# Kernel tuning notes

Measured on AMD Instinct MI355X. Metric: run time of the kernel, lower is better.

The kernel has to match this reference:

```python
import jax, jax.numpy as jnp
import numpy as np

B, S, E = 4, 2048, 768
H = 12
D = E // H  # 64

def setup_inputs() -> dict:
    key = jax.random.key(0)
    k_x, k_wqkv, k_wproj = jax.random.split(key, 3)
    x = jax.random.normal(k_x, (B, S, E), dtype=jnp.float32)
    w_qkv = jax.random.normal(k_wqkv, (E, 3 * E), dtype=jnp.float32) * 0.02
    b_qkv = jnp.zeros((3 * E,), dtype=jnp.float32)
    w_proj = jax.random.normal(k_wproj, (E, E), dtype=jnp.float32) * 0.02
    b_proj = jnp.zeros((E,), dtype=jnp.float32)
    return {"x": x, "w_qkv": w_qkv, "b_qkv": b_qkv, "w_proj": w_proj, "b_proj": b_proj}

def reference(x, w_qkv, b_qkv, w_proj, b_proj):
    # fused QKV projection: [B,S,E] -> [B,S,3E]
    qkv = jnp.einsum("bse,ef->bsf", x, w_qkv) + b_qkv
    qkv = qkv.reshape(B, S, 3, H, D)
    q, k, v = qkv[:, :, 0], qkv[:, :, 1], qkv[:, :, 2]  # [B,S,H,D]
    scale = 1.0 / jnp.sqrt(jnp.asarray(D, dtype=x.dtype))
    # causal scaled dot-product attention (explicit score matrix, as in module)
    scores = jnp.einsum("bshd,bthd->bhst", q, k) * scale  # [B,H,S,S]
    causal = jnp.tril(jnp.ones((S, S), dtype=bool))
    scores = jnp.where(causal, scores, jnp.finfo(scores.dtype).min)
    probs = jax.nn.softmax(scores, axis=-1)
    attn = jnp.einsum("bhst,bthd->bshd", probs, v).reshape(B, S, E)
    # output projection
    out = jnp.einsum("bse,ef->bsf", attn, w_proj) + b_proj
    return out
```

## Files before the change

### kernel.cpp

```cpp
#include <hip/hip_runtime.h>

#define SDIM 2048
#define EDIM 768
#define HDIM 12
#define DDIM 64
#define BDIM 4
#define MROWS (BDIM * SDIM)
#define NQKV (3 * EDIM)
#define NBH (BDIM * HDIM)
#define NTILE 32
#define NPAIR 16

typedef __attribute__((ext_vector_type(8))) short s16x8;
typedef __attribute__((ext_vector_type(4))) float f32x4;
typedef __attribute__((ext_vector_type(2))) unsigned int u32x2;

__device__ __forceinline__ short f2b(float x) {
  union { float f; unsigned u; } v; v.f = x;
  unsigned r = v.u + 0x7fffu + ((v.u >> 16) & 1u);
  return (short)(r >> 16);
}

__device__ __forceinline__ unsigned cvtpk(float lo, float hi) {
  unsigned r;
  asm volatile("v_cvt_pk_bf16_f32 %0, %1, %2" : "=v"(r) : "v"(lo), "v"(hi));
  return r;
}

__device__ __forceinline__ float fexp2(float x) {
  float r;
  asm("v_exp_f32 %0, %1" : "=v"(r) : "v"(x));
  return r;
}

__device__ __forceinline__ void gld16(const void* g, void* l) {
  __builtin_amdgcn_global_load_lds(
      (const __attribute__((address_space(1))) unsigned int*)g,
      (__attribute__((address_space(3))) unsigned int*)l, 16, 0, 0);
}

__global__ __launch_bounds__(256) void preproc(
    const float* __restrict__ x, const float* __restrict__ wqkv,
    const float* __restrict__ wproj, short* __restrict__ xb,
    short* __restrict__ wqkvt, short* __restrict__ wprojt) {
  int bid = blockIdx.x;
  if (bid < 1536) {
    int i = bid * 256 + threadIdx.x;
    const int n4 = MROWS * EDIM / 4;
    for (; i < n4; i += 1536 * 256) {
      float4 v = ((const float4*)x)[i];
      short4 o;
      o.x = f2b(v.x); o.y = f2b(v.y); o.z = f2b(v.z); o.w = f2b(v.w);
      ((short4*)xb)[i] = o;
    }
    return;
  }
  const float* in; short* out; int K, N, t;
  if (bid < 1536 + 1728) { t = bid - 1536; in = wqkv; out = wqkvt; K = EDIM; N = NQKV; }
  else { t = bid - 1536 - 1728; in = wproj; out = wprojt; K = EDIM; N = EDIM; }
  const int ntx = N / 32;
  int n0 = (t % ntx) * 32, k0 = (t / ntx) * 32;
  __shared__ float tb[32][33];
  int tx = threadIdx.x & 31, ty = threadIdx.x >> 5;
#pragma unroll
  for (int i = 0; i < 4; ++i)
    tb[ty + 8 * i][tx] = in[(size_t)(k0 + ty + 8 * i) * N + n0 + tx];
  __syncthreads();
#pragma unroll
  for (int i = 0; i < 4; ++i)
    out[(size_t)(n0 + ty + 8 * i) * K + k0 + tx] = f2b(tb[tx][ty + 8 * i]);
}

__global__ __launch_bounds__(256) void gemm_qkv(
    const short* __restrict__ A, const short* __restrict__ Bt,
    const float* __restrict__ bias, short* __restrict__ qout,
    short* __restrict__ kout, short* __restrict__ vout) {
  __shared__ char lds[3][16384];
  const int tid = threadIdx.x;
  const int l = tid & 63, w = tid >> 6;
  const int lr = l & 15, g = l >> 4;
  const int K = EDIM;

  const int chunk = gridDim.x >> 3;
  const int sid = (blockIdx.x & 7) * chunk + (blockIdx.x >> 3);
  const int ntx = NQKV >> 7;
  const int bm = (sid / ntx) * 128, bn = (sid % ntx) * 128;
  const int wm = w >> 1, wn = w & 1;

  const int srow = w * 32 + (l >> 2);
  const int sc8 = (((l & 3) ^ ((l >> 3) & 3)) << 3);
  const short* Ap0 = A + (size_t)(bm + srow) * K + sc8;
  const short* Bp0 = Bt + (size_t)(bn + srow) * K + sc8;

  f32x4 acc[4][4];
  const f32x4 z4 = {0.f, 0.f, 0.f, 0.f};
#pragma unroll
  for (int m = 0; m < 4; ++m)
#pragma unroll
    for (int n = 0; n < 4; ++n) acc[m][n] = z4;

#define STAGE(dst, t)                          \
  {                                            \
    char* Ad = (dst) + w * 2048;               \
    const short* Ap = Ap0 + (t) * 32;          \
    const short* Bp = Bp0 + (t) * 32;          \
    gld16(Ap, Ad);                             \
    gld16(Ap + 16 * K, Ad + 1024);             \
    gld16(Bp, Ad + 8192);                      \
    gld16(Bp + 16 * K, Ad + 9216);             \
  }

  const int nt = K >> 5;
  STAGE(lds[0], 0);
  STAGE(lds[1], 1);
  asm volatile("s_waitcnt vmcnt(4)" ::: "memory");
  __builtin_amdgcn_s_barrier();

  const int swz = ((lr >> 1) & 3) << 4;
  int bc = 0;
  for (int t = 0; t < nt; ++t) {
    if (t + 2 < nt) {
      int bs = bc + 2; if (bs >= 3) bs -= 3;
      STAGE(lds[bs], t + 2);
    }
    const char* Ab = lds[bc];
    const char* Bb = lds[bc] + 8192;
    s16x8 af[4], bfr[4];
#pragma unroll
    for (int m = 0; m < 4; ++m)
      af[m] = *(const s16x8*)(Ab + (wm * 64 + m * 16 + lr) * 64 + ((g << 4) ^ swz));
#pragma unroll
    for (int n = 0; n < 4; ++n)
      bfr[n] = *(const s16x8*)(Bb + (wn * 64 + n * 16 + lr) * 64 + ((g << 4) ^ swz));
    __builtin_amdgcn_s_setprio(1);
#pragma unroll
    for (int m = 0; m < 4; ++m)
#pragma unroll
      for (int n = 0; n < 4; ++n)
        acc[m][n] = __builtin_amdgcn_mfma_f32_16x16x32_bf16(af[m], bfr[n],
                                                            acc[m][n], 0, 0, 0);
    __builtin_amdgcn_s_setprio(0);
    if (t + 2 < nt) {
      asm volatile("s_waitcnt vmcnt(4)" ::: "memory");
      __builtin_amdgcn_s_barrier();
    } else if (t + 1 < nt) {
      asm volatile("s_waitcnt vmcnt(0)" ::: "memory");
      __builtin_amdgcn_s_barrier();
    }
    if (++bc == 3) bc = 0;
  }
#undef STAGE

#pragma unroll
  for (int m = 0; m < 4; ++m) {
    int rbase = bm + wm * 64 + m * 16 + g * 4;
#pragma unroll
    for (int n = 0; n < 4; ++n) {
      int col = bn + wn * 64 + n * 16 + lr;
      float bv = bias[col];
      int which = (col >= 1536) ? 2 : (col >= 768 ? 1 : 0);
      int rem = col - which * 768;
      int h = rem >> 6, d = rem & 63;
#pragma unroll
      for (int i = 0; i < 4; ++i) {
        int r = rbase + i;
        int bb = r >> 11, s = r & 2047;
        short o = f2b(acc[m][n][i] + bv);
        size_t bh = (size_t)bb * HDIM + h;
        if (which == 0)      qout[(bh * SDIM + s) * DDIM + d] = o;
        else if (which == 1) kout[(bh * SDIM + s) * DDIM + d] = o;
        else                 vout[(bh * DDIM + d) * SDIM + s] = o;
      }
    }
  }
}

__global__ __launch_bounds__(256) void gemm_proj(
    const short* __restrict__ A, const short* __restrict__ Bt,
    const float* __restrict__ bias, int M, int N, int K,
    float* __restrict__ fout) {
  __shared__ char lds[3][16384];
  const int tid = threadIdx.x;
  const int l = tid & 63, w = tid >> 6;
  const int lr = l & 15, g = l >> 4;

  const int chunk = gridDim.x >> 3;
  const int sid = (blockIdx.x & 7) * chunk + (blockIdx.x >> 3);
  const int ntx = N >> 7;
  const int bm = (sid / ntx) * 128, bn = (sid % ntx) * 128;
  const int wm = w >> 1, wn = w & 1;

  const int srow = w * 32 + (l >> 2);
  const int sc8 = (((l & 3) ^ ((l >> 3) & 3)) << 3);
  const short* Ap0 = A + (size_t)(bm + srow) * K + sc8;
  const short* Bp0 = Bt + (size_t)(bn + srow) * K + sc8;

  f32x4 acc[4][4];
  const f32x4 z4 = {0.f, 0.f, 0.f, 0.f};
#pragma unroll
  for (int m = 0; m < 4; ++m)
#pragma unroll
    for (int n = 0; n < 4; ++n) acc[m][n] = z4;

#define STAGE(dst, t)                          \
  {                                            \
    char* Ad = (dst) + w * 2048;               \
    const short* Ap = Ap0 + (t) * 32;          \
    const short* Bp = Bp0 + (t) * 32;          \
    gld16(Ap, Ad);                             \
    gld16(Ap + 16 * K, Ad + 1024);             \
    gld16(Bp, Ad + 8192);                      \
    gld16(Bp + 16 * K, Ad + 9216);             \
  }

  const int nt = K >> 5;
  STAGE(lds[0], 0);
  STAGE(lds[1], 1);
  asm volatile("s_waitcnt vmcnt(4)" ::: "memory");
  __builtin_amdgcn_s_barrier();

  const int swz = ((lr >> 1) & 3) << 4;
  int bc = 0;
  for (int t = 0; t < nt; ++t) {
    if (t + 2 < nt) {
      int bs = bc + 2; if (bs >= 3) bs -= 3;
      STAGE(lds[bs], t + 2);
    }
    const char* Ab = lds[bc];
    const char* Bb = lds[bc] + 8192;
    s16x8 af[4], bfr[4];
#pragma unroll
    for (int m = 0; m < 4; ++m)
      af[m] = *(const s16x8*)(Ab + (wm * 64 + m * 16 + lr) * 64 + ((g << 4) ^ swz));
#pragma unroll
    for (int n = 0; n < 4; ++n)
      bfr[n] = *(const s16x8*)(Bb + (wn * 64 + n * 16 + lr) * 64 + ((g << 4) ^ swz));
    __builtin_amdgcn_s_setprio(1);
#pragma unroll
    for (int m = 0; m < 4; ++m)
#pragma unroll
      for (int n = 0; n < 4; ++n)
        acc[m][n] = __builtin_amdgcn_mfma_f32_16x16x32_bf16(af[m], bfr[n],
                                                            acc[m][n], 0, 0, 0);
    __builtin_amdgcn_s_setprio(0);
    if (t + 2 < nt) {
      asm volatile("s_waitcnt vmcnt(4)" ::: "memory");
      __builtin_amdgcn_s_barrier();
    } else if (t + 1 < nt) {
      asm volatile("s_waitcnt vmcnt(0)" ::: "memory");
      __builtin_amdgcn_s_barrier();
    }
    if (++bc == 3) bc = 0;
  }
#undef STAGE

#pragma unroll
  for (int m = 0; m < 4; ++m) {
    int rbase = bm + wm * 64 + m * 16 + g * 4;
#pragma unroll
    for (int n = 0; n < 4; ++n) {
      int col = bn + wn * 64 + n * 16 + lr;
      float bv = bias[col];
#pragma unroll
      for (int i = 0; i < 4; ++i)
        fout[(size_t)(rbase + i) * N + col] = acc[m][n][i] + bv;
    }
  }
}

__global__ __launch_bounds__(256, 3) void attn_mfma4(
    const short* __restrict__ qb, const short* __restrict__ kb,
    const short* __restrict__ vb, short* __restrict__ ao) {
  __shared__ short kvbuf[2][8192];
  __shared__ short pstrip[4][1024];

  const int tid = threadIdx.x;
  const int l = tid & 63, w = tid >> 6;
  const int lr = l & 15, g = l >> 4;
  const int swz = (lr & 7) << 4;

  const int lin = blockIdx.x;
  const int xcd = lin & 7;
  const int idx = lin >> 3;
  const int bh = xcd * 6 + (idx >> 4);
  const int pair = idx & 15;
  const int tiles[2] = {NTILE - 1 - pair, pair};

  const int b = bh / HDIM, h = bh % HDIM;
  const size_t base = (size_t)bh * SDIM * DDIM;

  const int srow = w * 16 + (l >> 3);
  const int sc = (l & 7) ^ (srow & 7);
  const size_t koff0 = (size_t)srow * DDIM + sc * 8;
  const size_t koff1 = (size_t)(srow + 8) * DDIM + sc * 8;
  const size_t voff0 = (size_t)srow * SDIM + sc * 8;
  const size_t voff1 = (size_t)(srow + 8) * SDIM + sc * 8;

  const float SC = 0.125f * 1.4426950408889634f;
  char* sw = (char*)pstrip[w];

#define KVSTAGE(buf_, kt_)                                        \
  {                                                               \
    char* kd = (char*)kvbuf[buf_] + w * 2048;                     \
    const short* kp = kb + base + (size_t)(kt_) * 64 * DDIM;      \
    const short* vp = vb + base + (size_t)(kt_) * 64;             \
    gld16(kp + koff0, kd);                                        \
    gld16(kp + koff1, kd + 1024);                                 \
    gld16(vp + voff0, kd + 8192);                                 \
    gld16(vp + voff1, kd + 9216);                                 \
  }

  for (int half = 0; half < 2; ++half) {
    const int tile = tiles[half];
    const int q0w = tile * 64 + w * 16;

    s16x8 qa[2];
#pragma unroll
    for (int s = 0; s < 2; ++s)
      qa[s] = *(const s16x8*)(qb + base + (size_t)(q0w + lr) * DDIM + s * 32 + g * 8);

    const f32x4 z4 = {0.f, 0.f, 0.f, 0.f};
    f32x4 acco[4];
#pragma unroll
    for (int nd = 0; nd < 4; ++nd) acco[nd] = z4;
    float mrun = -1e30f, lsum = 0.f;

    KVSTAGE(0, 0);
    {
      const int t1 = (tile >= 1) ? 1 : 0;
      KVSTAGE(1, t1);
    }

    for (int kt = 0; kt <= tile; ++kt) {
      if (kt < tile) asm volatile("s_waitcnt vmcnt(4)" ::: "memory");
      else           asm volatile("s_waitcnt vmcnt(0)" ::: "memory");
      __builtin_amdgcn_s_barrier();

      const char* Kb = (const char*)kvbuf[kt & 1];
      const char* Vb = Kb + 8192;

      f32x4 sacc[4];
#pragma unroll
      for (int nt = 0; nt < 4; ++nt) sacc[nt] = z4;
      __builtin_amdgcn_s_setprio(1);
#pragma unroll
      for (int s = 0; s < 2; ++s)
#pragma unroll
        for (int nt = 0; nt < 4; ++nt) {
          s16x8 kf = *(const s16x8*)(Kb + nt * 2048 + lr * 128 +
                                     ((s * 64 + g * 16) ^ swz));
          sacc[nt] = __builtin_amdgcn_mfma_f32_16x16x32_bf16(kf, qa[s],
                                                             sacc[nt], 0, 0, 0);
        }
      __builtin_amdgcn_s_setprio(0);

      if (kt == tile) {
        const int rloc = w * 16 + lr;
#pragma unroll
        for (int nt = 0; nt < 4; ++nt)
#pragma unroll
          for (int i = 0; i < 4; ++i)
            if (nt * 16 + g * 4 + i > rloc) sacc[nt][i] = -1e30f;
      }

      float t0 = fmaxf(fmaxf(sacc[0][0], sacc[0][1]), fmaxf(sacc[0][2], sacc[0][3]));
      float t1 = fmaxf(fmaxf(sacc[1][0], sacc[1][1]), fmaxf(sacc[1][2], sacc[1][3]));
      float t2 = fmaxf(fmaxf(sacc[2][0], sacc[2][1]), fmaxf(sacc[2][2], sacc[2][3]));
      float t3 = fmaxf(fmaxf(sacc[3][0], sacc[3][1]), fmaxf(sacc[3][2], sacc[3][3]));
      float pmax = fmaxf(fmaxf(t0, t1), fmaxf(t2, t3));
      pmax = fmaxf(pmax, __shfl_xor(pmax, 16, 64));
      pmax = fmaxf(pmax, __shfl_xor(pmax, 32, 64));

      if (__any(pmax > mrun + 44.0f)) {
        float nm = fmaxf(mrun, pmax);
        float al = fexp2((mrun - nm) * SC);
        lsum *= al;
#pragma unroll
        for (int nd = 0; nd < 4; ++nd)
#pragma unroll
          for (int i = 0; i < 4; ++i) acco[nd][i] *= al;
        mrun = nm;
      }

      const float msc = mrun * SC;
#pragma unroll
      for (int nt = 0; nt < 4; ++nt) {
        float p0 = fexp2(__builtin_fmaf(sacc[nt][0], SC, -msc));
        float p1 = fexp2(__builtin_fmaf(sacc[nt][1], SC, -msc));
        float p2 = fexp2(__builtin_fmaf(sacc[nt][2], SC, -msc));
        float p3 = fexp2(__builtin_fmaf(sacc[nt][3], SC, -msc));
        lsum += (p0 + p1) + (p2 + p3);
        u32x2 pk = {cvtpk(p0, p1), cvtpk(p2, p3)};
        *(u32x2*)(sw + lr * 128 + (((nt * 32 + g * 8) ^ swz))) = pk;
      }

      __builtin_amdgcn_s_setprio(1);
#pragma unroll
      for (int s = 0; s < 2; ++s) {
        s16x8 pf = *(const s16x8*)(sw + lr * 128 + ((s * 64 + g * 16) ^ swz));
#pragma unroll
        for (int nd = 0; nd < 4; ++nd) {
          s16x8 vf = *(const s16x8*)(Vb + nd * 2048 + lr * 128 +
                                     ((s * 64 + g * 16) ^ swz));
          acco[nd] = __builtin_amdgcn_mfma_f32_16x16x32_bf16(vf, pf,
                                                             acco[nd], 0, 0, 0);
        }
      }
      __builtin_amdgcn_s_setprio(0);

      __builtin_amdgcn_s_barrier();
      if (kt + 2 <= tile) KVSTAGE(kt & 1, kt + 2);
    }

    lsum += __shfl_xor(lsum, 16, 64);
    lsum += __shfl_xor(lsum, 32, 64);
    float inv = 1.0f / lsum;
    size_t orow = ((size_t)b * SDIM + q0w + lr) * EDIM + h * DDIM;
#pragma unroll
    for (int nd = 0; nd < 4; ++nd) {
      unsigned lo = cvtpk(acco[nd][0] * inv, acco[nd][1] * inv);
      unsigned hi = cvtpk(acco[nd][2] * inv, acco[nd][3] * inv);
      *(unsigned*)(ao + orow + nd * 16 + g * 4) = lo;
      *(unsigned*)(ao + orow + nd * 16 + g * 4 + 2) = hi;
    }
  }
#undef KVSTAGE
}

extern "C" void kernel_launch(void* const* d_in, const int* in_sizes, int n_in,
                              void* d_out, int out_size, void* d_ws,
                              size_t ws_size, hipStream_t stream) {
  const float* x = (const float*)d_in[0];
  const float* w_qkv = (const float*)d_in[1];
  const float* b_qkv = (const float*)d_in[2];
  const float* w_proj = (const float*)d_in[3];
  const float* b_proj = (const float*)d_in[4];
  float* out = (float*)d_out;

  char* p = (char*)d_ws;
  short* xb = (short*)p;      p += (size_t)MROWS * EDIM * 2;
  short* wqkvt = (short*)p;   p += (size_t)NQKV * EDIM * 2;
  short* wprojt = (short*)p;  p += (size_t)EDIM * EDIM * 2;
  short* qbuf = (short*)p;    p += (size_t)NBH * SDIM * DDIM * 2;
  short* kbuf = (short*)p;    p += (size_t)NBH * SDIM * DDIM * 2;
  short* vbuf = (short*)p;    p += (size_t)NBH * SDIM * DDIM * 2;
  short* aob = (short*)p;     p += (size_t)MROWS * EDIM * 2;

  dim3 blk(256);
  preproc<<<dim3(1536 + 1728 + 576), blk, 0, stream>>>(x, w_qkv, w_proj, xb,
                                                       wqkvt, wprojt);
  gemm_qkv<<<dim3((MROWS / 128) * (NQKV / 128)), blk, 0, stream>>>(
      xb, wqkvt, b_qkv, qbuf, kbuf, vbuf);
  attn_mfma4<<<dim3(NPAIR * NBH), blk, 0, stream>>>(qbuf, kbuf, vbuf, aob);
  gemm_proj<<<dim3((MROWS / 128) * (EDIM / 128)), blk, 0, stream>>>(
      aob, wprojt, b_proj, MROWS, EDIM, EDIM, out);
}
```

Before: 136.9 us.

## Rewrite QKV GEMM as 256x256 tile, 8-wave kernel with deep LDS pipeline

Replaces the 128x128, 4-wave QKV projection GEMM with a 256x256-tile kernel that runs 512 threads (8 waves), each wave computing a 128x64 sub-tile. K is staged in 64-wide steps through 128KB of LDS, with half-tile stages interleaved between MFMA phases and explicit barriers. The goal is more data reuse per loaded byte and better overlap of global loads with MFMA work. The cost is a grid of only 288 blocks at one block per CU, which may leave CUs idle or unevenly loaded. It also adds higher register pressure and many more barriers.

```diff
diff --git a/kernel.cpp b/kernel.cpp
--- a/kernel.cpp
+++ b/kernel.cpp
@@ -71,19 +71,180 @@
     out[(size_t)(n0 + ty + 8 * i) * K + k0 + tx] = f2b(tb[tx][ty + 8 * i]);
 }
 
-__global__ __launch_bounds__(256) void gemm_qkv(
+__global__ __launch_bounds__(512, 1) void gemm_qkv8(
     const short* __restrict__ A, const short* __restrict__ Bt,
     const float* __restrict__ bias, short* __restrict__ qout,
     short* __restrict__ kout, short* __restrict__ vout) {
+  __shared__ char lds[131072];
+  const int tid = threadIdx.x;
+  const int l = tid & 63;
+  const int w = tid >> 6;
+  const int lr = l & 15, g = l >> 4;
+  const int K = EDIM;
+  const int nt = K >> 6;
+  const int nh = nt << 2;
+
+  const int chunk = gridDim.x >> 3;
+  const int sid = (blockIdx.x & 7) * chunk + (blockIdx.x >> 3);
+  const int ntx = NQKV >> 8;
+  const int bm = (sid / ntx) << 8;
+  const int bn = (sid % ntx) << 8;
+  const int wm = w >> 2, wn = w & 3;
+
+  const int srow = tid >> 2;
+  const int sck = ((tid & 3) ^ ((tid >> 3) & 3)) << 3;
+  const short* Ab = A + (size_t)(bm + srow) * K + sck;
+  const short* Bb = Bt + (size_t)(bn + srow) * K + sck;
+  char* dst0 = lds + tid * 16;
+
+#define STAGEH(i)                                                     \
+  {                                                                   \
+    char* d_ = dst0 + ((i) & 7) * 16384;                              \
+    const short* s_ = (((i) & 1) ? Bb : Ab) + ((i) >> 2) * 64 +       \
+                      (((i) >> 1) & 1) * 32;                          \
+    gld16(s_, d_);                                                    \
+    gld16(s_ + 128 * K, d_ + 8192);                                   \
+  }
+
+  f32x4 acc[8][4];
+  const f32x4 z4 = {0.f, 0.f, 0.f, 0.f};
+#pragma unroll
+  for (int mf = 0; mf < 8; ++mf)
+#pragma unroll
+    for (int nf = 0; nf < 4; ++nf) acc[mf][nf] = z4;
+
+  STAGEH(0); STAGEH(1); STAGEH(2); STAGEH(3);
+  asm volatile("s_waitcnt vmcnt(4)" ::: "memory");
+  STAGEH(4); STAGEH(5); STAGEH(6);
+  asm volatile("s_waitcnt vmcnt(6)" ::: "memory");
+  __builtin_amdgcn_s_barrier();
+
+  const int cg = (g << 4) ^ (((lr >> 1) & 3) << 4);
+  const int arow = (wm * 128 + lr) * 64;
+  const int brow = (wn * 64 + lr) * 64;
+
+  s16x8 a[4], b[4];
+
+#pragma unroll 2
+  for (int k = 0; k < nt; ++k) {
+    char* As0 = lds + ((k & 1) * 4 + 0) * 16384;
+    char* Bs0 = lds + ((k & 1) * 4 + 1) * 16384;
+    char* As1 = lds + ((k & 1) * 4 + 2) * 16384;
+    char* Bs1 = lds + ((k & 1) * 4 + 3) * 16384;
+    const int P = k << 2;
+
+#pragma unroll
+    for (int mf = 0; mf < 4; ++mf)
+      a[mf] = *(const s16x8*)(As0 + arow + mf * 1024 + cg);
+#pragma unroll
+    for (int nf = 0; nf < 4; ++nf)
+      b[nf] = *(const s16x8*)(Bs0 + brow + nf * 1024 + cg);
+    if (P + 7 < nh) STAGEH(P + 7);
+    __builtin_amdgcn_s_barrier();
+    asm volatile("s_waitcnt lgkmcnt(0)" ::: "memory");
+    __builtin_amdgcn_s_setprio(1);
+#pragma unroll
+    for (int mf = 0; mf < 4; ++mf)
+#pragma unroll
+      for (int nf = 0; nf < 4; ++nf)
+        acc[mf][nf] = __builtin_amdgcn_mfma_f32_16x16x32_bf16(a[mf], b[nf],
+                                                              acc[mf][nf], 0, 0, 0);
+    __builtin_amdgcn_s_setprio(0);
+    __builtin_amdgcn_s_barrier();
+
+#pragma unroll
+    for (int mf = 0; mf < 4; ++mf)
+      a[mf] = *(const s16x8*)(As0 + arow + (mf + 4) * 1024 + cg);
+    if (P + 8 < nh) STAGEH(P + 8);
+    __builtin_amdgcn_s_barrier();
+    asm volatile("s_waitcnt lgkmcnt(0)" ::: "memory");
+    __builtin_amdgcn_s_setprio(1);
+#pragma unroll
+    for (int mf = 0; mf < 4; ++mf)
+#pragma unroll
+      for (int nf = 0; nf < 4; ++nf)
+        acc[mf + 4][nf] = __builtin_amdgcn_mfma_f32_16x16x32_bf16(
+            a[mf], b[nf], acc[mf + 4][nf], 0, 0, 0);
+    __builtin_amdgcn_s_setprio(0);
+    __builtin_amdgcn_s_barrier();
+
+#pragma unroll
+    for (int mf = 0; mf < 4; ++mf)
+      a[mf] = *(const s16x8*)(As1 + arow + mf * 1024 + cg);
+#pragma unroll
+    for (int nf = 0; nf < 4; ++nf)
+      b[nf] = *(const s16x8*)(Bs1 + brow + nf * 1024 + cg);
+    if (P + 9 < nh) STAGEH(P + 9);
+    __builtin_amdgcn_s_barrier();
+    asm volatile("s_waitcnt lgkmcnt(0)" ::: "memory");
+    __builtin_amdgcn_s_setprio(1);
+#pragma unroll
+    for (int mf = 0; mf < 4; ++mf)
+#pragma unroll
+      for (int nf = 0; nf < 4; ++nf)
+        acc[mf][nf] = __builtin_amdgcn_mfma_f32_16x16x32_bf16(a[mf], b[nf],
+                                                              acc[mf][nf], 0, 0, 0);
+    __builtin_amdgcn_s_setprio(0);
+    __builtin_amdgcn_s_barrier();
+
+#pragma unroll
+    for (int mf = 0; mf < 4; ++mf)
+      a[mf] = *(const s16x8*)(As1 + arow + (mf + 4) * 1024 + cg);
+    if (P + 10 < nh) STAGEH(P + 10);
+    __builtin_amdgcn_s_barrier();
+    asm volatile("s_waitcnt lgkmcnt(0)" ::: "memory");
+    __builtin_amdgcn_s_setprio(1);
+#pragma unroll
+    for (int mf = 0; mf < 4; ++mf)
+#pragma unroll
+      for (int nf = 0; nf < 4; ++nf)
+        acc[mf + 4][nf] = __builtin_amdgcn_mfma_f32_16x16x32_bf16(
+            a[mf], b[nf], acc[mf + 4][nf], 0, 0, 0);
+    __builtin_amdgcn_s_setprio(0);
+    if (k + 1 < nt) {
+      if (k + 2 < nt) asm volatile("s_waitcnt vmcnt(6)" ::: "memory");
+      else            asm volatile("s_waitcnt vmcnt(0)" ::: "memory");
+      __builtin_amdgcn_s_barrier();
+    }
+  }
+#undef STAGEH
+
+#pragma unroll
+  for (int mf = 0; mf < 8; ++mf) {
+    int rbase = bm + wm * 128 + mf * 16 + g * 4;
+#pragma unroll
+    for (int nf = 0; nf < 4; ++nf) {
+      int col = bn + wn * 64 + nf * 16 + lr;
+      float bv = bias[col];
+      int which = (col >= 1536) ? 2 : (col >= 768 ? 1 : 0);
+      int rem = col - which * 768;
+      int h = rem >> 6, d = rem & 63;
+#pragma unroll
+      for (int i = 0; i < 4; ++i) {
+        int r = rbase + i;
+        int bb = r >> 11, s = r & 2047;
+        short o = f2b(acc[mf][nf][i] + bv);
+        size_t bh = (size_t)bb * HDIM + h;
+        if (which == 0)      qout[(bh * SDIM + s) * DDIM + d] = o;
+        else if (which == 1) kout[(bh * SDIM + s) * DDIM + d] = o;
+        else                 vout[(bh * DDIM + d) * SDIM + s] = o;
+      }
+    }
+  }
+}
+
+__global__ __launch_bounds__(256) void gemm_proj(
+    const short* __restrict__ A, const short* __restrict__ Bt,
+    const float* __restrict__ bias, int M, int N, int K,
+    float* __restrict__ fout) {
   __shared__ char lds[3][16384];
   const int tid = threadIdx.x;
   const int l = tid & 63, w = tid >> 6;
   const int lr = l & 15, g = l >> 4;
-  const int K = EDIM;
 
   const int chunk = gridDim.x >> 3;
   const int sid = (blockIdx.x & 7) * chunk + (blockIdx.x >> 3);
-  const int ntx = NQKV >> 7;
+  const int ntx = N >> 7;
   const int bm = (sid / ntx) * 128, bn = (sid % ntx) * 128;
   const int wm = w >> 1, wn = w & 1;
 
@@ -158,109 +319,6 @@
     for (int n = 0; n < 4; ++n) {
       int col = bn + wn * 64 + n * 16 + lr;
       float bv = bias[col];
-      int which = (col >= 1536) ? 2 : (col >= 768 ? 1 : 0);
-      int rem = col - which * 768;
-      int h = rem >> 6, d = rem & 63;
-#pragma unroll
-      for (int i = 0; i < 4; ++i) {
-        int r = rbase + i;
-        int bb = r >> 11, s = r & 2047;
-        short o = f2b(acc[m][n][i] + bv);
-        size_t bh = (size_t)bb * HDIM + h;
-        if (which == 0)      qout[(bh * SDIM + s) * DDIM + d] = o;
-        else if (which == 1) kout[(bh * SDIM + s) * DDIM + d] = o;
-        else                 vout[(bh * DDIM + d) * SDIM + s] = o;
-      }
-    }
-  }
-}
-
-__global__ __launch_bounds__(256) void gemm_proj(
-    const short* __restrict__ A, const short* __restrict__ Bt,
-    const float* __restrict__ bias, int M, int N, int K,
-    float* __restrict__ fout) {
-  __shared__ char lds[3][16384];
-  const int tid = threadIdx.x;
-  const int l = tid & 63, w = tid >> 6;
-  const int lr = l & 15, g = l >> 4;
-
-  const int chunk = gridDim.x >> 3;
-  const int sid = (blockIdx.x & 7) * chunk + (blockIdx.x >> 3);
-  const int ntx = N >> 7;
-  const int bm = (sid / ntx) * 128, bn = (sid % ntx) * 128;
-  const int wm = w >> 1, wn = w & 1;
-
-  const int srow = w * 32 + (l >> 2);
-  const int sc8 = (((l & 3) ^ ((l >> 3) & 3)) << 3);
-  const short* Ap0 = A + (size_t)(bm + srow) * K + sc8;
-  const short* Bp0 = Bt + (size_t)(bn + srow) * K + sc8;
-
-  f32x4 acc[4][4];
-  const f32x4 z4 = {0.f, 0.f, 0.f, 0.f};
-#pragma unroll
-  for (int m = 0; m < 4; ++m)
-#pragma unroll
-    for (int n = 0; n < 4; ++n) acc[m][n] = z4;
-
-#define STAGE(dst, t)                          \
-  {                                            \
-    char* Ad = (dst) + w * 2048;               \
-    const short* Ap = Ap0 + (t) * 32;          \
-    const short* Bp = Bp0 + (t) * 32;          \
-    gld16(Ap, Ad);                             \
-    gld16(Ap + 16 * K, Ad + 1024);             \
-    gld16(Bp, Ad + 8192);                      \
-    gld16(Bp + 16 * K, Ad + 9216);             \
-  }
-
-  const int nt = K >> 5;
-  STAGE(lds[0], 0);
-  STAGE(lds[1], 1);
-  asm volatile("s_waitcnt vmcnt(4)" ::: "memory");
-  __builtin_amdgcn_s_barrier();
-
-  const int swz = ((lr >> 1) & 3) << 4;
-  int bc = 0;
-  for (int t = 0; t < nt; ++t) {
-    if (t + 2 < nt) {
-      int bs = bc + 2; if (bs >= 3) bs -= 3;
-      STAGE(lds[bs], t + 2);
-    }
-    const char* Ab = lds[bc];
-    const char* Bb = lds[bc] + 8192;
-    s16x8 af[4], bfr[4];
-#pragma unroll
-    for (int m = 0; m < 4; ++m)
-      af[m] = *(const s16x8*)(Ab + (wm * 64 + m * 16 + lr) * 64 + ((g << 4) ^ swz));
-#pragma unroll
-    for (int n = 0; n < 4; ++n)
-      bfr[n] = *(const s16x8*)(Bb + (wn * 64 + n * 16 + lr) * 64 + ((g << 4) ^ swz));
-    __builtin_amdgcn_s_setprio(1);
-#pragma unroll
-    for (int m = 0; m < 4; ++m)
-#pragma unroll
-      for (int n = 0; n < 4; ++n)
-        acc[m][n] = __builtin_amdgcn_mfma_f32_16x16x32_bf16(af[m], bfr[n],
-                                                            acc[m][n], 0, 0, 0);
-    __builtin_amdgcn_s_setprio(0);
-    if (t + 2 < nt) {
-      asm volatile("s_waitcnt vmcnt(4)" ::: "memory");
-      __builtin_amdgcn_s_barrier();
-    } else if (t + 1 < nt) {
-      asm volatile("s_waitcnt vmcnt(0)" ::: "memory");
-      __builtin_amdgcn_s_barrier();
-    }
-    if (++bc == 3) bc = 0;
-  }
-#undef STAGE
-
-#pragma unroll
-  for (int m = 0; m < 4; ++m) {
-    int rbase = bm + wm * 64 + m * 16 + g * 4;
-#pragma unroll
-    for (int n = 0; n < 4; ++n) {
-      int col = bn + wn * 64 + n * 16 + lr;
-      float bv = bias[col];
 #pragma unroll
       for (int i = 0; i < 4; ++i)
         fout[(size_t)(rbase + i) * N + col] = acc[m][n][i] + bv;
@@ -449,7 +507,7 @@
   dim3 blk(256);
   preproc<<<dim3(1536 + 1728 + 576), blk, 0, stream>>>(x, w_qkv, w_proj, xb,
                                                        wqkvt, wprojt);
-  gemm_qkv<<<dim3((MROWS / 128) * (NQKV / 128)), blk, 0, stream>>>(
+  gemm_qkv8<<<dim3((MROWS / 256) * (NQKV / 256)), dim3(512), 0, stream>>>(
       xb, wqkvt, b_qkv, qbuf, kbuf, vbuf);
   attn_mfma4<<<dim3(NPAIR * NBH), blk, 0, stream>>>(qbuf, kbuf, vbuf, aob);
   gemm_proj<<<dim3((MROWS / 128) * (EDIM / 128)), blk, 0, stream>>>(
```

New measurement: 156.1 us. 14.0% more time.

## Pre-swizzle QKV GEMM operands into MFMA fragment layout and drop LDS staging

Applied to the files above, without the earlier changes.

The preprocessing kernel now writes x and w_qkv in bf16 directly in a per-16x32 tile fragment order, laid out so each lane's MFMA operand is one contiguous 16-byte chunk. The QKV GEMM then loads fragments straight from global memory into registers, dropping the LDS triple buffer, the barriers and the swizzle. This removes LDS traffic and synchronisation from the QKV GEMM. In exchange it loses software-pipelined prefetch and relies on cache and occupancy to hide global latency. Operands are also re-read from L2 by each wave rather than shared through LDS.

```diff
diff --git a/kernel.cpp b/kernel.cpp
--- a/kernel.cpp
+++ b/kernel.cpp
@@ -10,6 +10,7 @@
 #define NBH (BDIM * HDIM)
 #define NTILE 32
 #define NPAIR 16
+#define NKT 24
 
 typedef __attribute__((ext_vector_type(8))) short s16x8;
 typedef __attribute__((ext_vector_type(4))) float f32x4;
@@ -43,47 +44,124 @@
     const float* __restrict__ x, const float* __restrict__ wqkv,
     const float* __restrict__ wproj, short* __restrict__ xb,
     short* __restrict__ wqkvt, short* __restrict__ wprojt) {
-  int bid = blockIdx.x;
-  if (bid < 1536) {
-    int i = bid * 256 + threadIdx.x;
-    const int n4 = MROWS * EDIM / 4;
-    for (; i < n4; i += 1536 * 256) {
-      float4 v = ((const float4*)x)[i];
-      short4 o;
-      o.x = f2b(v.x); o.y = f2b(v.y); o.z = f2b(v.z); o.w = f2b(v.w);
-      ((short4*)xb)[i] = o;
-    }
+  const int bid = blockIdx.x;
+  const int tid = threadIdx.x;
+  const int l = tid & 63, w = tid >> 6;
+  const int lr = l & 15, g = l >> 4;
+  if (bid < 3072) {
+    const int T = bid * 4 + w;
+    const int rt = T / NKT, kt = T % NKT;
+    const float* src = x + (size_t)(rt * 16 + lr) * EDIM + kt * 32 + g * 8;
+    float4 v0 = *(const float4*)(src);
+    float4 v1 = *(const float4*)(src + 4);
+    s16x8 o;
+    o[0] = f2b(v0.x); o[1] = f2b(v0.y); o[2] = f2b(v0.z); o[3] = f2b(v0.w);
+    o[4] = f2b(v1.x); o[5] = f2b(v1.y); o[6] = f2b(v1.z); o[7] = f2b(v1.w);
+    *(s16x8*)(xb + (size_t)T * 512 + l * 8) = o;
     return;
   }
-  const float* in; short* out; int K, N, t;
-  if (bid < 1536 + 1728) { t = bid - 1536; in = wqkv; out = wqkvt; K = EDIM; N = NQKV; }
-  else { t = bid - 1536 - 1728; in = wproj; out = wprojt; K = EDIM; N = EDIM; }
-  const int ntx = N / 32;
-  int n0 = (t % ntx) * 32, k0 = (t / ntx) * 32;
+  if (bid < 3072 + 864) {
+    const int T = (bid - 3072) * 4 + w;
+    const int ct = T / NKT, kt = T % NKT;
+    s16x8 o;
+#pragma unroll
+    for (int j = 0; j < 8; ++j)
+      o[j] = f2b(wqkv[(size_t)(kt * 32 + g * 8 + j) * NQKV + ct * 16 + lr]);
+    *(s16x8*)(wqkvt + (size_t)T * 512 + l * 8) = o;
+    return;
+  }
+  const int t = bid - 3072 - 864;
+  const int n0 = (t % 24) * 32, k0 = (t / 24) * 32;
   __shared__ float tb[32][33];
-  int tx = threadIdx.x & 31, ty = threadIdx.x >> 5;
+  int tx = tid & 31, ty = tid >> 5;
 #pragma unroll
   for (int i = 0; i < 4; ++i)
-    tb[ty + 8 * i][tx] = in[(size_t)(k0 + ty + 8 * i) * N + n0 + tx];
+    tb[ty + 8 * i][tx] = wproj[(size_t)(k0 + ty + 8 * i) * EDIM + n0 + tx];
   __syncthreads();
 #pragma unroll
   for (int i = 0; i < 4; ++i)
-    out[(size_t)(n0 + ty + 8 * i) * K + k0 + tx] = f2b(tb[tx][ty + 8 * i]);
+    wprojt[(size_t)(n0 + ty + 8 * i) * EDIM + k0 + tx] = f2b(tb[tx][ty + 8 * i]);
 }
 
 __global__ __launch_bounds__(256) void gemm_qkv(
     const short* __restrict__ A, const short* __restrict__ Bt,
     const float* __restrict__ bias, short* __restrict__ qout,
     short* __restrict__ kout, short* __restrict__ vout) {
+  const int tid = threadIdx.x;
+  const int l = tid & 63, w = tid >> 6;
+  const int lr = l & 15, g = l >> 4;
+
+  const int chunk = gridDim.x >> 3;
+  const int sid = (blockIdx.x & 7) * chunk + (blockIdx.x >> 3);
+  const int ntx = NQKV >> 7;
+  const int bm = (sid / ntx) * 128, bn = (sid % ntx) * 128;
+  const int wm = w >> 1, wn = w & 1;
+
+  const short* Ab = A + ((size_t)(bm >> 4) + wm * 4) * NKT * 512 + l * 8;
+  const short* Bb = Bt + ((size_t)(bn >> 4) + wn * 4) * NKT * 512 + l * 8;
+
+  f32x4 acc[4][4];
+  const f32x4 z4 = {0.f, 0.f, 0.f, 0.f};
+#pragma unroll
+  for (int m = 0; m < 4; ++m)
+#pragma unroll
+    for (int n = 0; n < 4; ++n) acc[m][n] = z4;
+
+#pragma unroll 4
+  for (int kt = 0; kt < NKT; ++kt) {
+    s16x8 af[4], bf[4];
+#pragma unroll
+    for (int m = 0; m < 4; ++m)
+      af[m] = *(const s16x8*)(Ab + (size_t)m * NKT * 512 + kt * 512);
+#pragma unroll
+    for (int n = 0; n < 4; ++n)
+      bf[n] = *(const s16x8*)(Bb + (size_t)n * NKT * 512 + kt * 512);
+    __builtin_amdgcn_s_setprio(1);
+#pragma unroll
+    for (int m = 0; m < 4; ++m)
+#pragma unroll
+      for (int n = 0; n < 4; ++n)
+        acc[m][n] = __builtin_amdgcn_mfma_f32_16x16x32_bf16(af[m], bf[n],
+                                                            acc[m][n], 0, 0, 0);
+    __builtin_amdgcn_s_setprio(0);
+  }
+
+#pragma unroll
+  for (int m = 0; m < 4; ++m) {
+    int rbase = bm + wm * 64 + m * 16 + g * 4;
+#pragma unroll
+    for (int n = 0; n < 4; ++n) {
+      int col = bn + wn * 64 + n * 16 + lr;
+      float bv = bias[col];
+      int which = (col >= 1536) ? 2 : (col >= 768 ? 1 : 0);
+      int rem = col - which * 768;
+      int h = rem >> 6, d = rem & 63;
+#pragma unroll
+      for (int i = 0; i < 4; ++i) {
+        int r = rbase + i;
+        int bb = r >> 11, s = r & 2047;
+        short o = f2b(acc[m][n][i] + bv);
+        size_t bh = (size_t)bb * HDIM + h;
+        if (which == 0)      qout[(bh * SDIM + s) * DDIM + d] = o;
+        else if (which == 1) kout[(bh * SDIM + s) * DDIM + d] = o;
+        else                 vout[(bh * DDIM + d) * SDIM + s] = o;
+      }
+    }
+  }
+}
+
+__global__ __launch_bounds__(256) void gemm_proj(
+    const short* __restrict__ A, const short* __restrict__ Bt,
+    const float* __restrict__ bias, int M, int N, int K,
+    float* __restrict__ fout) {
   __shared__ char lds[3][16384];
   const int tid = threadIdx.x;
   const int l = tid & 63, w = tid >> 6;
   const int lr = l & 15, g = l >> 4;
-  const int K = EDIM;
 
   const int chunk = gridDim.x >> 3;
   const int sid = (blockIdx.x & 7) * chunk + (blockIdx.x >> 3);
-  const int ntx = NQKV >> 7;
+  const int ntx = N >> 7;
   const int bm = (sid / ntx) * 128, bn = (sid % ntx) * 128;
   const int wm = w >> 1, wn = w & 1;
 
@@ -158,109 +236,6 @@
     for (int n = 0; n < 4; ++n) {
       int col = bn + wn * 64 + n * 16 + lr;
       float bv = bias[col];
-      int which = (col >= 1536) ? 2 : (col >= 768 ? 1 : 0);
-      int rem = col - which * 768;
-      int h = rem >> 6, d = rem & 63;
-#pragma unroll
-      for (int i = 0; i < 4; ++i) {
-        int r = rbase + i;
-        int bb = r >> 11, s = r & 2047;
-        short o = f2b(acc[m][n][i] + bv);
-        size_t bh = (size_t)bb * HDIM + h;
-        if (which == 0)      qout[(bh * SDIM + s) * DDIM + d] = o;
-        else if (which == 1) kout[(bh * SDIM + s) * DDIM + d] = o;
-        else                 vout[(bh * DDIM + d) * SDIM + s] = o;
-      }
-    }
-  }
-}
-
-__global__ __launch_bounds__(256) void gemm_proj(
-    const short* __restrict__ A, const short* __restrict__ Bt,
-    const float* __restrict__ bias, int M, int N, int K,
-    float* __restrict__ fout) {
-  __shared__ char lds[3][16384];
-  const int tid = threadIdx.x;
-  const int l = tid & 63, w = tid >> 6;
-  const int lr = l & 15, g = l >> 4;
-
-  const int chunk = gridDim.x >> 3;
-  const int sid = (blockIdx.x & 7) * chunk + (blockIdx.x >> 3);
-  const int ntx = N >> 7;
-  const int bm = (sid / ntx) * 128, bn = (sid % ntx) * 128;
-  const int wm = w >> 1, wn = w & 1;
-
-  const int srow = w * 32 + (l >> 2);
-  const int sc8 = (((l & 3) ^ ((l >> 3) & 3)) << 3);
-  const short* Ap0 = A + (size_t)(bm + srow) * K + sc8;
-  const short* Bp0 = Bt + (size_t)(bn + srow) * K + sc8;
-
-  f32x4 acc[4][4];
-  const f32x4 z4 = {0.f, 0.f, 0.f, 0.f};
-#pragma unroll
-  for (int m = 0; m < 4; ++m)
-#pragma unroll
-    for (int n = 0; n < 4; ++n) acc[m][n] = z4;
-
-#define STAGE(dst, t)                          \
-  {                                            \
-    char* Ad = (dst) + w * 2048;               \
-    const short* Ap = Ap0 + (t) * 32;          \
-    const short* Bp = Bp0 + (t) * 32;          \
-    gld16(Ap, Ad);                             \
-    gld16(Ap + 16 * K, Ad + 1024);             \
-    gld16(Bp, Ad + 8192);                      \
-    gld16(Bp + 16 * K, Ad + 9216);             \
-  }
-
-  const int nt = K >> 5;
-  STAGE(lds[0], 0);
-  STAGE(lds[1], 1);
-  asm volatile("s_waitcnt vmcnt(4)" ::: "memory");
-  __builtin_amdgcn_s_barrier();
-
-  const int swz = ((lr >> 1) & 3) << 4;
-  int bc = 0;
-  for (int t = 0; t < nt; ++t) {
-    if (t + 2 < nt) {
-      int bs = bc + 2; if (bs >= 3) bs -= 3;
-      STAGE(lds[bs], t + 2);
-    }
-    const char* Ab = lds[bc];
-    const char* Bb = lds[bc] + 8192;
-    s16x8 af[4], bfr[4];
-#pragma unroll
-    for (int m = 0; m < 4; ++m)
-      af[m] = *(const s16x8*)(Ab + (wm * 64 + m * 16 + lr) * 64 + ((g << 4) ^ swz));
-#pragma unroll
-    for (int n = 0; n < 4; ++n)
-      bfr[n] = *(const s16x8*)(Bb + (wn * 64 + n * 16 + lr) * 64 + ((g << 4) ^ swz));
-    __builtin_amdgcn_s_setprio(1);
-#pragma unroll
-    for (int m = 0; m < 4; ++m)
-#pragma unroll
-      for (int n = 0; n < 4; ++n)
-        acc[m][n] = __builtin_amdgcn_mfma_f32_16x16x32_bf16(af[m], bfr[n],
-                                                            acc[m][n], 0, 0, 0);
-    __builtin_amdgcn_s_setprio(0);
-    if (t + 2 < nt) {
-      asm volatile("s_waitcnt vmcnt(4)" ::: "memory");
-      __builtin_amdgcn_s_barrier();
-    } else if (t + 1 < nt) {
-      asm volatile("s_waitcnt vmcnt(0)" ::: "memory");
-      __builtin_amdgcn_s_barrier();
-    }
-    if (++bc == 3) bc = 0;
-  }
-#undef STAGE
-
-#pragma unroll
-  for (int m = 0; m < 4; ++m) {
-    int rbase = bm + wm * 64 + m * 16 + g * 4;
-#pragma unroll
-    for (int n = 0; n < 4; ++n) {
-      int col = bn + wn * 64 + n * 16 + lr;
-      float bv = bias[col];
 #pragma unroll
       for (int i = 0; i < 4; ++i)
         fout[(size_t)(rbase + i) * N + col] = acc[m][n][i] + bv;
@@ -447,8 +422,8 @@
   short* aob = (short*)p;     p += (size_t)MROWS * EDIM * 2;
 
   dim3 blk(256);
-  preproc<<<dim3(1536 + 1728 + 576), blk, 0, stream>>>(x, w_qkv, w_proj, xb,
-                                                       wqkvt, wprojt);
+  preproc<<<dim3(3072 + 864 + 576), blk, 0, stream>>>(x, w_qkv, w_proj, xb,
+                                                      wqkvt, wprojt);
   gemm_qkv<<<dim3((MROWS / 128) * (NQKV / 128)), blk, 0, stream>>>(
       xb, wqkvt, b_qkv, qbuf, kbuf, vbuf);
   attn_mfma4<<<dim3(NPAIR * NBH), blk, 0, stream>>>(qbuf, kbuf, vbuf, aob);
```

Result: slower. 145.4 us (+6.2%).

## Retile QKV GEMM to one 256x288 tile per CU with wave-specialized loads

Applied to the files above, without the earlier changes.

The QKV projection GEMM now uses 512-thread blocks, each computing a 256x288 output tile, giving exactly 256 blocks (one per CU) instead of many 128x128 tiles. Two waves stage A and six waves stage B through a 4-slot LDS ring, with per-wave vmcnt waits. Each wave computes 4x9 MFMA fragments. The aim is more data reuse per LDS load, fewer global reloads and no tail wave. In exchange it uses large LDS and register footprints at occupancy 1 and has less latency hiding.

```diff
diff --git a/kernel.cpp b/kernel.cpp
--- a/kernel.cpp
+++ b/kernel.cpp
@@ -71,19 +71,143 @@
     out[(size_t)(n0 + ty + 8 * i) * K + k0 + tx] = f2b(tb[tx][ty + 8 * i]);
 }
 
-__global__ __launch_bounds__(256) void gemm_qkv(
+__global__ __launch_bounds__(512, 1) void gemm_qkv(
     const short* __restrict__ A, const short* __restrict__ Bt,
     const float* __restrict__ bias, short* __restrict__ qout,
     short* __restrict__ kout, short* __restrict__ vout) {
+  __shared__ char lds[4][34816];
+  const int tid = threadIdx.x;
+  const int l = tid & 63, w = tid >> 6;
+  const int lr = l & 15, g = l >> 4;
+  const int K = EDIM;
+  const int wu = __builtin_amdgcn_readfirstlane(w);
+
+  const int chunk = gridDim.x >> 3;
+  const int sid = (blockIdx.x & 7) * chunk + (blockIdx.x >> 3);
+  const int bm = (sid >> 3) << 8;
+  const int bn = (sid & 7) * 288;
+  const int wm = w >> 1, wn = w & 1;
+
+  int soff[8], dbase[8];
+  const short* sb;
+  if (wu < 2) {
+    sb = A + (size_t)bm * K;
+#pragma unroll
+    for (int j = 0; j < 8; ++j) {
+      int c = j * 128 + w * 64 + l;
+      int row = c >> 2, sc = (c & 3) ^ ((c >> 3) & 3);
+      soff[j] = row * K + sc * 8;
+      dbase[j] = c * 16;
+    }
+  } else {
+    sb = Bt + (size_t)bn * K;
+#pragma unroll
+    for (int j = 0; j < 3; ++j) {
+      int c = j * 384 + (w - 2) * 64 + l;
+      int row = c >> 2, sc = (c & 3) ^ ((c >> 3) & 3);
+      soff[j] = row * K + sc * 8;
+      dbase[j] = 16384 + c * 16;
+    }
+  }
+
+#define STAGE(s_, t_)                                            \
+  {                                                              \
+    char* d_ = lds[(s_)];                                        \
+    if (wu < 2) {                                                \
+      _Pragma("unroll")                                          \
+      for (int j = 0; j < 8; ++j)                                \
+        gld16(sb + soff[j] + (t_) * 32, d_ + dbase[j]);          \
+    } else {                                                     \
+      _Pragma("unroll")                                          \
+      for (int j = 0; j < 3; ++j)                                \
+        gld16(sb + soff[j] + (t_) * 32, d_ + dbase[j]);          \
+    }                                                            \
+  }
+#define WAITN()                                                  \
+  {                                                              \
+    if (wu < 2) asm volatile("s_waitcnt vmcnt(8)" ::: "memory"); \
+    else        asm volatile("s_waitcnt vmcnt(3)" ::: "memory"); \
+  }
+
+  f32x4 acc[4][9];
+  const f32x4 z4 = {0.f, 0.f, 0.f, 0.f};
+#pragma unroll
+  for (int mf = 0; mf < 4; ++mf)
+#pragma unroll
+    for (int nf = 0; nf < 9; ++nf) acc[mf][nf] = z4;
+
+  const int NS = K >> 5;
+  STAGE(0, 0);
+  STAGE(1, 1);
+  WAITN();
+  __builtin_amdgcn_s_barrier();
+
+  const int cg = (g << 4) ^ (((lr >> 1) & 3) << 4);
+  for (int t = 0; t < NS; ++t) {
+    if (t + 2 < NS) STAGE((t + 2) & 3, t + 2);
+    const char* sl = lds[t & 3];
+    s16x8 af[4], bf[9];
+#pragma unroll
+    for (int mf = 0; mf < 4; ++mf)
+      af[mf] = *(const s16x8*)(sl + (wm * 64 + mf * 16 + lr) * 64 + cg);
+#pragma unroll
+    for (int nf = 0; nf < 9; ++nf)
+      bf[nf] = *(const s16x8*)(sl + 16384 + (wn * 144 + nf * 16 + lr) * 64 + cg);
+    __builtin_amdgcn_s_setprio(1);
+#pragma unroll
+    for (int mf = 0; mf < 4; ++mf)
+#pragma unroll
+      for (int nf = 0; nf < 9; ++nf)
+        acc[mf][nf] = __builtin_amdgcn_mfma_f32_16x16x32_bf16(af[mf], bf[nf],
+                                                              acc[mf][nf], 0, 0, 0);
+    __builtin_amdgcn_s_setprio(0);
+    if (t + 2 < NS) {
+      WAITN();
+      __builtin_amdgcn_s_barrier();
+    } else if (t + 1 < NS) {
+      asm volatile("s_waitcnt vmcnt(0)" ::: "memory");
+      __builtin_amdgcn_s_barrier();
+    }
+  }
+#undef STAGE
+#undef WAITN
+
+#pragma unroll
+  for (int mf = 0; mf < 4; ++mf) {
+    int rbase = bm + wm * 64 + mf * 16 + g * 4;
+#pragma unroll
+    for (int nf = 0; nf < 9; ++nf) {
+      int col = bn + wn * 144 + nf * 16 + lr;
+      float bv = bias[col];
+      int which = (col >= 1536) ? 2 : (col >= 768 ? 1 : 0);
+      int rem = col - which * 768;
+      int h = rem >> 6, d = rem & 63;
+#pragma unroll
+      for (int i = 0; i < 4; ++i) {
+        int r = rbase + i;
+        int bb = r >> 11, s = r & 2047;
+        short o = f2b(acc[mf][nf][i] + bv);
+        size_t bh = (size_t)bb * HDIM + h;
+        if (which == 0)      qout[(bh * SDIM + s) * DDIM + d] = o;
+        else if (which == 1) kout[(bh * SDIM + s) * DDIM + d] = o;
+        else                 vout[(bh * DDIM + d) * SDIM + s] = o;
+      }
+    }
+  }
+}
+
+__global__ __launch_bounds__(256) void gemm_proj(
+    const short* __restrict__ A, const short* __restrict__ Bt,
+    const float* __restrict__ bias, int M, int N, int K,
+    float* __restrict__ fout) {
   __shared__ char lds[3][16384];
   const int tid = threadIdx.x;
   const int l = tid & 63, w = tid >> 6;
   const int lr = l & 15, g = l >> 4;
-  const int K = EDIM;
 
   const int chunk = gridDim.x >> 3;
   const int sid = (blockIdx.x & 7) * chunk + (blockIdx.x >> 3);
-  const int ntx = NQKV >> 7;
+  const int ntx = N >> 7;
   const int bm = (sid / ntx) * 128, bn = (sid % ntx) * 128;
   const int wm = w >> 1, wn = w & 1;
 
@@ -158,109 +282,6 @@
     for (int n = 0; n < 4; ++n) {
       int col = bn + wn * 64 + n * 16 + lr;
       float bv = bias[col];
-      int which = (col >= 1536) ? 2 : (col >= 768 ? 1 : 0);
-      int rem = col - which * 768;
-      int h = rem >> 6, d = rem & 63;
-#pragma unroll
-      for (int i = 0; i < 4; ++i) {
-        int r = rbase + i;
-        int bb = r >> 11, s = r & 2047;
-        short o = f2b(acc[m][n][i] + bv);
-        size_t bh = (size_t)bb * HDIM + h;
-        if (which == 0)      qout[(bh * SDIM + s) * DDIM + d] = o;
-        else if (which == 1) kout[(bh * SDIM + s) * DDIM + d] = o;
-        else                 vout[(bh * DDIM + d) * SDIM + s] = o;
-      }
-    }
-  }
-}
-
-__global__ __launch_bounds__(256) void gemm_proj(
-    const short* __restrict__ A, const short* __restrict__ Bt,
-    const float* __restrict__ bias, int M, int N, int K,
-    float* __restrict__ fout) {
-  __shared__ char lds[3][16384];
-  const int tid = threadIdx.x;
-  const int l = tid & 63, w = tid >> 6;
-  const int lr = l & 15, g = l >> 4;
-
-  const int chunk = gridDim.x >> 3;
-  const int sid = (blockIdx.x & 7) * chunk + (blockIdx.x >> 3);
-  const int ntx = N >> 7;
-  const int bm = (sid / ntx) * 128, bn = (sid % ntx) * 128;
-  const int wm = w >> 1, wn = w & 1;
-
-  const int srow = w * 32 + (l >> 2);
-  const int sc8 = (((l & 3) ^ ((l >> 3) & 3)) << 3);
-  const short* Ap0 = A + (size_t)(bm + srow) * K + sc8;
-  const short* Bp0 = Bt + (size_t)(bn + srow) * K + sc8;
-
-  f32x4 acc[4][4];
-  const f32x4 z4 = {0.f, 0.f, 0.f, 0.f};
-#pragma unroll
-  for (int m = 0; m < 4; ++m)
-#pragma unroll
-    for (int n = 0; n < 4; ++n) acc[m][n] = z4;
-
-#define STAGE(dst, t)                          \
-  {                                            \
-    char* Ad = (dst) + w * 2048;               \
-    const short* Ap = Ap0 + (t) * 32;          \
-    const short* Bp = Bp0 + (t) * 32;          \
-    gld16(Ap, Ad);                             \
-    gld16(Ap + 16 * K, Ad + 1024);             \
-    gld16(Bp, Ad + 8192);                      \
-    gld16(Bp + 16 * K, Ad + 9216);             \
-  }
-
-  const int nt = K >> 5;
-  STAGE(lds[0], 0);
-  STAGE(lds[1], 1);
-  asm volatile("s_waitcnt vmcnt(4)" ::: "memory");
-  __builtin_amdgcn_s_barrier();
-
-  const int swz = ((lr >> 1) & 3) << 4;
-  int bc = 0;
-  for (int t = 0; t < nt; ++t) {
-    if (t + 2 < nt) {
-      int bs = bc + 2; if (bs >= 3) bs -= 3;
-      STAGE(lds[bs], t + 2);
-    }
-    const char* Ab = lds[bc];
-    const char* Bb = lds[bc] + 8192;
-    s16x8 af[4], bfr[4];
-#pragma unroll
-    for (int m = 0; m < 4; ++m)
-      af[m] = *(const s16x8*)(Ab + (wm * 64 + m * 16 + lr) * 64 + ((g << 4) ^ swz));
-#pragma unroll
-    for (int n = 0; n < 4; ++n)
-      bfr[n] = *(const s16x8*)(Bb + (wn * 64 + n * 16 + lr) * 64 + ((g << 4) ^ swz));
-    __builtin_amdgcn_s_setprio(1);
-#pragma unroll
-    for (int m = 0; m < 4; ++m)
-#pragma unroll
-      for (int n = 0; n < 4; ++n)
-        acc[m][n] = __builtin_amdgcn_mfma_f32_16x16x32_bf16(af[m], bfr[n],
-                                                            acc[m][n], 0, 0, 0);
-    __builtin_amdgcn_s_setprio(0);
-    if (t + 2 < nt) {
-      asm volatile("s_waitcnt vmcnt(4)" ::: "memory");
-      __builtin_amdgcn_s_barrier();
-    } else if (t + 1 < nt) {
-      asm volatile("s_waitcnt vmcnt(0)" ::: "memory");
-      __builtin_amdgcn_s_barrier();
-    }
-    if (++bc == 3) bc = 0;
-  }
-#undef STAGE
-
-#pragma unroll
-  for (int m = 0; m < 4; ++m) {
-    int rbase = bm + wm * 64 + m * 16 + g * 4;
-#pragma unroll
-    for (int n = 0; n < 4; ++n) {
-      int col = bn + wn * 64 + n * 16 + lr;
-      float bv = bias[col];
 #pragma unroll
       for (int i = 0; i < 4; ++i)
         fout[(size_t)(rbase + i) * N + col] = acc[m][n][i] + bv;
@@ -449,8 +470,8 @@
   dim3 blk(256);
   preproc<<<dim3(1536 + 1728 + 576), blk, 0, stream>>>(x, w_qkv, w_proj, xb,
                                                        wqkvt, wprojt);
-  gemm_qkv<<<dim3((MROWS / 128) * (NQKV / 128)), blk, 0, stream>>>(
-      xb, wqkvt, b_qkv, qbuf, kbuf, vbuf);
+  gemm_qkv<<<dim3(256), dim3(512), 0, stream>>>(xb, wqkvt, b_qkv, qbuf, kbuf,
+                                                vbuf);
   attn_mfma4<<<dim3(NPAIR * NBH), blk, 0, stream>>>(qbuf, kbuf, vbuf, aob);
   gemm_proj<<<dim3((MROWS / 128) * (EDIM / 128)), blk, 0, stream>>>(
       aob, wprojt, b_proj, MROWS, EDIM, EDIM, out);
```

After: 138.2 us. About the same (+1.0%).
